# Optimization experiments

Measured on AMD Instinct MI355X. Metric: run time of the kernel, lower is better.

The kernel has to match this reference:

```python
import jax, jax.numpy as jnp
import numpy as np

EMB = 64
HEADS = 8
POOL = 2          # instruction_pool_size
TOK = 10          # tokens_per_instruction
CAP = 32          # max_capped_distances per axis -> tables have 2*CAP-1 rows


def setup_inputs() -> dict:
    key = jax.random.key(0)
    ks = jax.random.split(key, 8)
    scale = float(np.sqrt(6.0 / (TOK + EMB)))  # xavier-ish; exact init irrelevant for math
    return {
        "enc_cross": jax.random.uniform(ks[0], (POOL, TOK, EMB), jnp.float32, -scale, scale),
        "enc_h": jax.random.uniform(ks[1], (2 * CAP - 1, EMB), jnp.float32, -scale, scale),
        "enc_w": jax.random.uniform(ks[2], (2 * CAP - 1, EMB), jnp.float32, -scale, scale),
        "enc_d": jax.random.uniform(ks[3], (2 * CAP - 1, EMB), jnp.float32, -scale, scale),
        "w_cross": jax.random.uniform(ks[4], (HEADS, EMB), jnp.float32, -scale, scale),
        "w_h": jax.random.uniform(ks[5], (HEADS, EMB), jnp.float32, -scale, scale),
        "w_w": jax.random.uniform(ks[6], (HEADS, EMB), jnp.float32, -scale, scale),
        "w_d": jax.random.uniform(ks[7], (HEADS, EMB), jnp.float32, -scale, scale),
        "dim_q": 4116,
        "dim_k": 4116,
        "dim_i": 20,
        "dim_h": 16,
        "dim_w": 16,
        "dim_d": 16,
    }


def _rel_embed(n, table):
    # table: [2*cap-1, emb]; returns gathered relative-position embeddings [n, n, emb]
    cap = (table.shape[0] + 1) // 2
    r = jnp.arange(n)
    idx = jnp.clip(r[None, :] - r[:, None] + cap - 1, 0, 2 * cap - 2)
    return table[idx]


def reference(enc_cross, enc_h, enc_w, enc_d, w_cross, w_h, w_w, w_d,
              dim_q, dim_k, dim_i, dim_h, dim_w, dim_d):
    tok = enc_cross.shape[1]
    emb = enc_cross.shape[-1]
    heads = w_cross.shape[0]
    inv_temperature = emb ** -0.5

    # instruction -> content embeddings: first n_cat tables concatenated (label_indices=None path)
    n_cat = dim_i // tok
    cross_emb = enc_cross[:n_cat].reshape(1, n_cat * tok, emb)  # [1, dim_i, emb]

    row_e = _rel_embed(dim_h, enc_h)  # [h, h, emb]
    col_e = _rel_embed(dim_w, enc_w)  # [w, w, emb]
    dep_e = _rel_embed(dim_d, enc_d)  # [d, d, emb]

    cross_s = jnp.einsum('hc,bnc->bhn', w_cross, cross_emb)        # [1, heads, dim_i]
    row_s = jnp.einsum('hc,nmc->hnm', w_h, row_e)[None]            # [1, heads, h, h]
    col_s = jnp.einsum('hc,nmc->hnm', w_w, col_e)[None]            # [1, heads, w, w]
    dep_s = jnp.einsum('hc,nmc->hnm', w_d, dep_e)[None]            # [1, heads, d, d]

    # broadcast-add over (i j k | l m n) -> [1, heads, h, w, d, h, w, d]
    content = (row_s[:, :, :, None, None, :, None, None]
               + col_s[:, :, None, :, None, None, :, None]
               + dep_s[:, :, None, None, :, None, None, :]) / 3.0
    S = dim_h * dim_w * dim_d
    content = content.reshape(1, heads, S, S)

    scores = jnp.zeros((1, heads, dim_q, dim_k), jnp.float32)
    # instruction bias block: rows dim_i:, cols :dim_i
    scores = scores.at[:, :, dim_i:, :dim_i].set(
        jnp.broadcast_to(cross_s[:, :, None, :], (1, heads, dim_q - dim_i, dim_i)))
    # content bias block: rows dim_i:, cols dim_i:
    scores = scores.at[:, :, dim_i:, dim_i:].set(content)
    return scores * inv_temperature
```

## Files before the change

### kernel.cpp

```cpp
#include <hip/hip_runtime.h>


#define EMB 64
#define NHEADS 8
#define DIM_I 20
#define DIM_Q 4116
#define NCHUNK 1029
#define OFF_ROW 160
#define OFF_COL (160 + 2048)
#define OFF_DEP (160 + 4096)
#define N_DOTS 6304

typedef float v4f __attribute__((ext_vector_type(4)));

__global__ __launch_bounds__(256) void tables_kernel(
    const float* __restrict__ enc_cross,
    const float* __restrict__ enc_h,
    const float* __restrict__ enc_w,
    const float* __restrict__ enc_d,
    const float* __restrict__ w_cross,
    const float* __restrict__ w_h,
    const float* __restrict__ w_w,
    const float* __restrict__ w_d,
    float* __restrict__ tabs)
{
    const int wid  = (blockIdx.x * 256 + threadIdx.x) >> 6;
    const int lane = threadIdx.x & 63;
    if (wid >= N_DOTS) return;

    const float* wv;
    const float* ev;
    float scale;
    int outidx;
    if (wid < 160) {
        const int h = wid / DIM_I;
        const int n = wid % DIM_I;
        wv = w_cross + h * EMB;
        ev = enc_cross + n * EMB;
        scale = 0.125f;
        outidx = wid;
    } else {
        const int u = wid - 160;
        const int table = u >> 11;
        const int v = u & 2047;
        const int h = v >> 8;
        const int i = (v >> 4) & 15;
        const int l = v & 15;
        const int ridx = l - i + 31;
        if (table == 0)      { wv = w_h + h * EMB; ev = enc_h + ridx * EMB; }
        else if (table == 1) { wv = w_w + h * EMB; ev = enc_w + ridx * EMB; }
        else                 { wv = w_d + h * EMB; ev = enc_d + ridx * EMB; }
        scale = 0.125f / 3.0f;
        outidx = 160 + u;
    }

    float p = wv[lane] * ev[lane];
    #pragma unroll
    for (int off = 32; off >= 1; off >>= 1)
        p += __shfl_xor(p, off, 64);
    if (lane == 0) tabs[outidx] = p * scale;
}

__global__ __launch_bounds__(256) void fill_kernel(
    const float* __restrict__ tabs, float* __restrict__ out)
{
    const int h   = blockIdx.y;
    const int r   = blockIdx.x;
    const int tid = threadIdx.x;
    float* outh = out + (size_t)h * DIM_Q * DIM_Q;

    if (r >= 256) {
        v4f* p = (v4f*)outh + (size_t)(r - 256) * 10290;
        const v4f z = {0.f, 0.f, 0.f, 0.f};
        for (int t = tid; t < 10290; t += 256)
            __builtin_nontemporal_store(z, p + t);
        return;
    }

    __shared__ __align__(16) float Base[256];
    __shared__ __align__(16) float dep[256];
    __shared__ float cross20[DIM_I];

    const int i = r >> 4;
    const int j = r & 15;
    Base[tid] = tabs[OFF_ROW + h * 256 + i * 16 + (tid >> 4)]
              + tabs[OFF_COL + h * 256 + j * 16 + (tid & 15)];
    dep[tid] = tabs[OFF_DEP + h * 256 + tid];
    if (tid < DIM_I) cross20[tid] = tabs[h * DIM_I + tid];
    __syncthreads();

    const int q0 = DIM_I + i * 256 + j * 16;
    for (int kk = 0; kk < 16; ++kk) {
        v4f* rowp = (v4f*)(outh + (size_t)(q0 + kk) * DIM_Q);
        const float* ds = dep + kk * 16;
        for (int t = tid; t < NCHUNK; t += 256) {
            v4f v;
            if (t < 5) {
                const int k0 = 4 * t;
                v.x = cross20[k0 + 0];
                v.y = cross20[k0 + 1];
                v.z = cross20[k0 + 2];
                v.w = cross20[k0 + 3];
            } else {
                const int c0 = 4 * t - DIM_I;
                const float b = Base[c0 >> 4];
                const v4f d = *(const v4f*)(ds + (c0 & 15));
                v = d + b;
            }
            __builtin_nontemporal_store(v, rowp + t);
        }
    }
}

extern "C" void kernel_launch(void* const* d_in, const int* in_sizes, int n_in,
                              void* d_out, int out_size, void* d_ws, size_t ws_size,
                              hipStream_t stream)
{
    const float* enc_cross = (const float*)d_in[0];
    const float* enc_h     = (const float*)d_in[1];
    const float* enc_w     = (const float*)d_in[2];
    const float* enc_d     = (const float*)d_in[3];
    const float* w_cross   = (const float*)d_in[4];
    const float* w_h       = (const float*)d_in[5];
    const float* w_w       = (const float*)d_in[6];
    const float* w_d       = (const float*)d_in[7];

    float* tabs = (float*)d_ws;

    tables_kernel<<<dim3((N_DOTS * 64 + 255) / 256), dim3(256), 0, stream>>>(
        enc_cross, enc_h, enc_w, enc_d, w_cross, w_h, w_w, w_d, tabs);

    fill_kernel<<<dim3(258, NHEADS), dim3(256), 0, stream>>>(
        tabs, (float*)d_out);
}
```

Before: 611.1 us.

## Restructure fill kernel per-wave rows with register-held col/dep sums, plain stores

The fill kernel now gives each wave four output rows. Each lane keeps the column+depth partial sum in registers and adds a broadcast row value for each of 16 unrolled 256-float segments, replacing the per-element shared-memory Base/dep lookups and the cross-vs-content branch. Nontemporal stores are replaced with ordinary stores, for both the content rows and the zero region. The tables kernel writes its output by wave id directly, which gives the same indices as before. Plain stores may pollute the cache on a write-only output of several hundred MB.

```diff
diff --git a/kernel.cpp b/kernel.cpp
--- a/kernel.cpp
+++ b/kernel.cpp
@@ -5,7 +5,6 @@
 #define NHEADS 8
 #define DIM_I 20
 #define DIM_Q 4116
-#define NCHUNK 1029
 #define OFF_ROW 160
 #define OFF_COL (160 + 2048)
 #define OFF_DEP (160 + 4096)
@@ -31,14 +30,12 @@
     const float* wv;
     const float* ev;
     float scale;
-    int outidx;
     if (wid < 160) {
         const int h = wid / DIM_I;
         const int n = wid % DIM_I;
         wv = w_cross + h * EMB;
         ev = enc_cross + n * EMB;
         scale = 0.125f;
-        outidx = wid;
     } else {
         const int u = wid - 160;
         const int table = u >> 11;
@@ -51,14 +48,13 @@
         else if (table == 1) { wv = w_w + h * EMB; ev = enc_w + ridx * EMB; }
         else                 { wv = w_d + h * EMB; ev = enc_d + ridx * EMB; }
         scale = 0.125f / 3.0f;
-        outidx = 160 + u;
     }
 
     float p = wv[lane] * ev[lane];
     #pragma unroll
     for (int off = 32; off >= 1; off >>= 1)
         p += __shfl_xor(p, off, 64);
-    if (lane == 0) tabs[outidx] = p * scale;
+    if (lane == 0) tabs[wid] = p * scale;
 }
 
 __global__ __launch_bounds__(256) void fill_kernel(
@@ -72,42 +68,38 @@
     if (r >= 256) {
         v4f* p = (v4f*)outh + (size_t)(r - 256) * 10290;
         const v4f z = {0.f, 0.f, 0.f, 0.f};
-        for (int t = tid; t < 10290; t += 256)
-            __builtin_nontemporal_store(z, p + t);
+        for (int t = tid; t < 10290; t += 256) p[t] = z;
         return;
     }
 
-    __shared__ __align__(16) float Base[256];
-    __shared__ __align__(16) float dep[256];
-    __shared__ float cross20[DIM_I];
+    const int i    = r >> 4;
+    const int j    = r & 15;
+    const int lane = tid & 63;
+    const int wave = tid >> 6;
 
-    const int i = r >> 4;
-    const int j = r & 15;
-    Base[tid] = tabs[OFF_ROW + h * 256 + i * 16 + (tid >> 4)]
-              + tabs[OFF_COL + h * 256 + j * 16 + (tid & 15)];
-    dep[tid] = tabs[OFF_DEP + h * 256 + tid];
-    if (tid < DIM_I) cross20[tid] = tabs[h * DIM_I + tid];
+    __shared__ float A16[16];
+    __shared__ __align__(16) float C[256];
+    if (tid < 16) A16[tid] = tabs[OFF_ROW + h * 256 + i * 16 + tid];
+    C[tid] = tabs[OFF_DEP + h * 256 + tid];
+
+    const float vB = tabs[OFF_COL + h * 256 + j * 16 + (lane >> 2)];
+    v4f vcross = {0.f, 0.f, 0.f, 0.f};
+    if (lane < 5) vcross = *(const v4f*)(tabs + h * DIM_I + 4 * lane);
     __syncthreads();
 
     const int q0 = DIM_I + i * 256 + j * 16;
-    for (int kk = 0; kk < 16; ++kk) {
-        v4f* rowp = (v4f*)(outh + (size_t)(q0 + kk) * DIM_Q);
-        const float* ds = dep + kk * 16;
-        for (int t = tid; t < NCHUNK; t += 256) {
-            v4f v;
-            if (t < 5) {
-                const int k0 = 4 * t;
-                v.x = cross20[k0 + 0];
-                v.y = cross20[k0 + 1];
-                v.z = cross20[k0 + 2];
-                v.w = cross20[k0 + 3];
-            } else {
-                const int c0 = 4 * t - DIM_I;
-                const float b = Base[c0 >> 4];
-                const v4f d = *(const v4f*)(ds + (c0 & 15));
-                v = d + b;
-            }
-            __builtin_nontemporal_store(v, rowp + t);
+    for (int rr = 0; rr < 4; ++rr) {
+        const int kk = wave * 4 + rr;
+        float* rowp = outh + (size_t)(q0 + kk) * DIM_Q;
+        const v4f vC = *(const v4f*)(C + kk * 16 + ((lane * 4) & 15));
+        const v4f vBC = vC + vB;
+        if (lane < 5) *(v4f*)(rowp + 4 * lane) = vcross;
+        float* cp = rowp + DIM_I;
+        #pragma unroll
+        for (int s = 0; s < 16; ++s) {
+            const float As = A16[s];
+            v4f v = vBC + As;
+            *(v4f*)(cp + s * 256 + 4 * lane) = v;
         }
     }
 }
```

Result: faster. 569.2 us (-6.9%).
